# Kernel tuning notes

Measured on AMD Instinct MI355X. Metric: run time of the kernel, lower is better.

The kernel has to match this reference:

```python
import jax, jax.numpy as jnp
import numpy as np

B, Z, H, T = 256, 512, 1024, 512   # batch, z_size, hidden (conductor==decoder), num_tokens
L, N = 16, 16                      # num_levels, notes_per_bar


def setup_inputs() -> dict:
    key = jax.random.key(0)
    ks = jax.random.split(key, 16)
    s = 0.05  # weight init scale
    rn = lambda k, shp, sc=1.0: sc * jax.random.normal(k, shp, dtype=jnp.float32)
    return {
        "z": rn(ks[0], (B, L * N, 1, Z)),
        "dec_h0": rn(ks[1], (L, B, H)),
        "dec_c0": rn(ks[2], (L, B, H)),
        # linear_in (computed but unused by the original forward)
        "lin_in_W": rn(ks[3], (Z, Z), s), "lin_in_b": rn(ks[4], (Z,), s),
        # conductor LSTM (input Z -> hidden H), PyTorch gate order i,f,g,o
        "cond_Wih": rn(ks[5], (4 * H, Z), s), "cond_Whh": rn(ks[6], (4 * H, H), s),
        "cond_bih": rn(ks[7], (4 * H,), s), "cond_bhh": rn(ks[8], (4 * H,), s),
        # decoder LSTM (input T+H -> hidden H)
        "dec_Wih": rn(ks[9], (4 * H, T + H), s), "dec_Whh": rn(ks[10], (4 * H, H), s),
        "dec_bih": rn(ks[11], (4 * H,), s), "dec_bhh": rn(ks[12], (4 * H,), s),
        # output projection
        "out_W": rn(ks[13], (T, H), s), "out_b": rn(ks[14], (T,), s),
    }


def _lstm_cell(x, h, c, Wih, Whh, b):
    gates = x @ Wih.T + h @ Whh.T + b            # [B, 4H]
    i, f, g, o = jnp.split(gates, 4, axis=-1)
    c = jax.nn.sigmoid(f) * c + jax.nn.sigmoid(i) * jnp.tanh(g)
    h = jax.nn.sigmoid(o) * jnp.tanh(c)
    return h, c


def reference(z, dec_h0, dec_c0, lin_in_W, lin_in_b,
              cond_Wih, cond_Whh, cond_bih, cond_bhh,
              dec_Wih, dec_Whh, dec_bih, dec_bhh, out_W, out_b):
    Bsz = z.shape[0]
    Tt = out_b.shape[0]
    Hh = cond_Whh.shape[1]

    _unused = z @ lin_in_W.T + lin_in_b  # linear_in output is discarded in the source

    cond_b = cond_bih + cond_bhh
    dec_b = dec_bih + dec_bhh

    # conductor consumes z[:, L*level, 0, :] for each level
    z_lv = jnp.transpose(z[:, jnp.arange(L) * L, 0, :], (1, 0, 2))  # [L, B, Z]

    def level_step(carry, xs):
        ch, cc = carry
        zl, dh, dc = xs
        ch, cc = _lstm_cell(zl, ch, cc, cond_Wih, cond_Whh, cond_b)
        emb = ch  # [B, H], fixed conductor embedding for this bar

        def note_step(c2, _):
            note, dh2, dc2 = c2
            inp = jnp.concatenate([emb, note], axis=-1)  # [B, H+T]
            dh2, dc2 = _lstm_cell(inp, dh2, dc2, dec_Wih, dec_Whh, dec_b)
            out = jax.nn.sigmoid(dh2 @ out_W.T + out_b)  # [B, T]
            return (out, dh2, dc2), out

        note0 = jnp.zeros((Bsz, Tt), dtype=z.dtype)
        _, outs = jax.lax.scan(note_step, (note0, dh, dc), None, length=N)  # [N, B, T]
        return (ch, cc), outs

    h0 = jnp.zeros((Bsz, Hh), dtype=z.dtype)
    _, all_outs = jax.lax.scan(level_step, (h0, h0), (z_lv, dec_h0, dec_c0))  # [L, N, B, T]
    notes = jnp.transpose(all_outs, (2, 0, 1, 3)).reshape(Bsz, L * N, Tt)
    return notes
```

## Files before the change

### kernel.cpp

```cpp
#include <hip/hip_runtime.h>

typedef __bf16 bf16;
typedef __attribute__((ext_vector_type(8))) __bf16 bf16x8;
typedef __attribute__((ext_vector_type(4))) float f32x4;
typedef __attribute__((ext_vector_type(4))) unsigned short u16x4;

__device__ __forceinline__ void gload_lds16(const void* g, void* l) {
  __builtin_amdgcn_global_load_lds(
      (const __attribute__((address_space(1))) void*)g,
      (__attribute__((address_space(3))) void*)l, 16, 0, 0);
}

__device__ __forceinline__ float sigmoidf_(float x) { return 1.0f / (1.0f + expf(-x)); }

__device__ __forceinline__ float bf2f(unsigned short u) {
  union { unsigned int i; float f; } v;
  v.i = ((unsigned int)u) << 16;
  return v.f;
}
__device__ __forceinline__ unsigned short f2bfbits(float x) {
  union { bf16 b; unsigned short u; } v;
  v.b = (bf16)x;
  return v.u;
}

#define SB() __builtin_amdgcn_sched_barrier(0)
#define BAR()                          \
  do {                                 \
    SB();                              \
    __builtin_amdgcn_s_barrier();      \
    SB();                              \
  } while (0)

#define MFMA16(a, b, c) __builtin_amdgcn_mfma_f32_16x16x32_bf16(a, b, c, 0, 0, 0)

template<int MODE>
__global__ __launch_bounds__(512, 2)
void gemm8(const bf16* __restrict__ A, int lda,
           const bf16* __restrict__ Bw, int K,
           bf16* __restrict__ Cb,
           const bf16* __restrict__ X, const float* __restrict__ bias,
           float* __restrict__ cst, bf16* __restrict__ hout, int ldh) {
  extern __shared__ __align__(16) char smem_raw[];
  bf16* lsA = (bf16*)smem_raw;
  bf16* lsB = lsA + 2 * 16384;

  const int tid = threadIdx.x;
  const int lane = tid & 63;
  const int wave = tid >> 6;
  const int wm = wave >> 2, wn = wave & 3;

  const int bid = blockIdx.x;
  const int wgid = (bid & 7) * 32 + (bid >> 3);
  const int m0 = (wgid >> 4) * 256, n0 = (wgid & 15) * 256;

  const int nkt = K >> 6;

  const int srow = tid >> 3;
  const int csw = ((tid & 7) * 8) ^ ((srow & 7) << 3);
  const bf16* gA = A + (size_t)m0 * lda + csw;
  const bf16* gB = Bw + (size_t)n0 * K + csw;

  auto stageA = [&](int kt) {
    bf16* d = lsA + (kt & 1) * 16384 + tid * 8;
    const bf16* s = gA + (size_t)srow * lda + (size_t)kt * 64;
    gload_lds16(s, d);
    gload_lds16(s + (size_t)64 * lda, d + 4096);
    gload_lds16(s + (size_t)128 * lda, d + 8192);
    gload_lds16(s + (size_t)192 * lda, d + 12288);
  };
  auto stageB = [&](int kt) {
    bf16* d = lsB + (kt & 1) * 16384 + tid * 8;
    const bf16* s = gB + (size_t)srow * K + (size_t)kt * 64;
    gload_lds16(s, d);
    gload_lds16(s + (size_t)64 * K, d + 4096);
    gload_lds16(s + (size_t)128 * K, d + 8192);
    gload_lds16(s + (size_t)192 * K, d + 12288);
  };

  const int c0 = ((lane >> 4) * 8) ^ ((lane & 7) << 3);
  const int c1 = c0 ^ 32;
  const int abase = (wm * 128 + (lane & 15)) * 64;
  const int bbase = (wn * 64 + (lane & 15)) * 64;

  f32x4 acc[8][4] = {};

  stageA(0); stageB(0);
  if (nkt > 1) stageB(1);
  if (nkt > 1) asm volatile("s_waitcnt vmcnt(4)" ::: "memory");
  else         asm volatile("s_waitcnt vmcnt(0)" ::: "memory");
  BAR();

  for (int u = 0; u < nkt; ++u) {
    const int c = u & 1;
    const bf16* pA = lsA + c * 16384;
    const bf16* pB = lsB + c * 16384;
    bf16x8 avA[4], avB[4], avC[4], avD[4], bvA[4], bvB[4];

    if (u + 1 < nkt) stageA(u + 1);
#pragma unroll
    for (int f = 0; f < 4; ++f) avA[f] = *(const bf16x8*)&pA[abase + f * 1024 + c0];
#pragma unroll
    for (int g = 0; g < 4; ++g) bvA[g] = *(const bf16x8*)&pB[bbase + g * 1024 + c0];
#pragma unroll
    for (int f = 0; f < 4; ++f) avB[f] = *(const bf16x8*)&pA[abase + (f + 4) * 1024 + c0];
    BAR();
    __builtin_amdgcn_s_setprio(1);
#pragma unroll
    for (int f = 0; f < 4; ++f)
#pragma unroll
      for (int g = 0; g < 4; ++g)
        acc[f][g] = MFMA16(avA[f], bvA[g], acc[f][g]);
    __builtin_amdgcn_s_setprio(0);
    BAR();

#pragma unroll
    for (int f = 0; f < 4; ++f) avC[f] = *(const bf16x8*)&pA[abase + f * 1024 + c1];
#pragma unroll
    for (int g = 0; g < 4; ++g) bvB[g] = *(const bf16x8*)&pB[bbase + g * 1024 + c1];
    __builtin_amdgcn_s_setprio(1);
#pragma unroll
    for (int f = 0; f < 4; ++f)
#pragma unroll
      for (int g = 0; g < 4; ++g)
        acc[f + 4][g] = MFMA16(avB[f], bvA[g], acc[f + 4][g]);
    __builtin_amdgcn_s_setprio(0);
    BAR();

#pragma unroll
    for (int f = 0; f < 4; ++f) avD[f] = *(const bf16x8*)&pA[abase + (f + 4) * 1024 + c1];
    __builtin_amdgcn_s_setprio(1);
#pragma unroll
    for (int f = 0; f < 4; ++f)
#pragma unroll
      for (int g = 0; g < 4; ++g)
        acc[f][g] = MFMA16(avC[f], bvB[g], acc[f][g]);
    __builtin_amdgcn_s_setprio(0);
    BAR();

    if (u + 2 < nkt) stageB(u + 2);
    SB();
    __builtin_amdgcn_s_setprio(1);
#pragma unroll
    for (int f = 0; f < 4; ++f)
#pragma unroll
      for (int g = 0; g < 4; ++g)
        acc[f + 4][g] = MFMA16(avD[f], bvB[g], acc[f + 4][g]);
    __builtin_amdgcn_s_setprio(0);
    if (u + 2 < nkt)      asm volatile("s_waitcnt vmcnt(4)" ::: "memory");
    else if (u + 1 < nkt) asm volatile("s_waitcnt vmcnt(0)" ::: "memory");
    BAR();
  }

  const int jj = lane & 15;
  const int rb = m0 + wm * 128 + ((lane >> 4) << 2);
  const int q = (n0 >> 6) + wn;
  if constexpr (MODE == 0) {
#pragma unroll
    for (int f = 0; f < 8; ++f)
#pragma unroll
      for (int r = 0; r < 4; ++r) {
        u16x4 pk;
        pk[0] = f2bfbits(acc[f][0][r]);
        pk[1] = f2bfbits(acc[f][1][r]);
        pk[2] = f2bfbits(acc[f][2][r]);
        pk[3] = f2bfbits(acc[f][3][r]);
        *(u16x4*)&Cb[(size_t)(rb + f * 16 + r) * 4096 + q * 64 + jj * 4] = pk;
      }
  } else {
    const int j = q * 16 + jj;
    const f32x4 bq = *(const f32x4*)&bias[q * 64 + jj * 4];
#pragma unroll
    for (int f = 0; f < 8; ++f) {
#pragma unroll
      for (int r = 0; r < 4; ++r) {
        const int row = rb + f * 16 + r;
        const u16x4 xv = *(const u16x4*)&X[(size_t)row * 4096 + q * 64 + jj * 4];
        const float gi = acc[f][0][r] + bf2f(xv[0]) + bq[0];
        const float gf = acc[f][1][r] + bf2f(xv[1]) + bq[1];
        const float gg = acc[f][2][r] + bf2f(xv[2]) + bq[2];
        const float go = acc[f][3][r] + bf2f(xv[3]) + bq[3];
        const size_t ci = (size_t)row * 1024 + j;
        const float cn = sigmoidf_(gf) * cst[ci] + sigmoidf_(gi) * tanhf(gg);
        cst[ci] = cn;
        hout[(size_t)row * ldh + j] = (bf16)(sigmoidf_(go) * tanhf(cn));
      }
    }
  }
}

template<int BM, int BN, int WM, int WN, int MODE>
__global__ __launch_bounds__(WM * WN * 64)
void gemm_bt(const bf16* __restrict__ A, int lda,
             const bf16* __restrict__ Bw, int ldb,
             float* __restrict__ C, int ldc, int K,
             const float* __restrict__ outb, float* __restrict__ dout,
             bf16* __restrict__ anote, int nstep) {
  constexpr int BK = 64;
  constexpr int THREADS = WM * WN * 64;
  constexpr int SM = BM / WM, SN = BN / WN;
  constexpr int FM = SM / 16, FN = SN / 16;

  __shared__ __align__(16) bf16 lsA[BM * BK];
  __shared__ __align__(16) bf16 lsB[BN * BK];

  const int tid = threadIdx.x;
  const int lane = tid & 63;
  const int wave = tid >> 6;
  const int wm = wave / WN, wn = wave % WN;
  const int m0 = blockIdx.y * BM;
  const int n0 = blockIdx.x * BN;

  f32x4 acc[FM][FN] = {};

  const bf16* gA = A + (size_t)m0 * lda;
  const bf16* gB = Bw + (size_t)n0 * ldb;

  for (int k0 = 0; k0 < K; k0 += BK) {
#pragma unroll
    for (int i = 0; i < (BM * 8) / THREADS; ++i) {
      int idx = i * THREADS + tid;
      gload_lds16(gA + (size_t)(idx >> 3) * lda + k0 + (idx & 7) * 8, &lsA[idx * 8]);
    }
#pragma unroll
    for (int i = 0; i < (BN * 8) / THREADS; ++i) {
      int idx = i * THREADS + tid;
      gload_lds16(gB + (size_t)(idx >> 3) * ldb + k0 + (idx & 7) * 8, &lsB[idx * 8]);
    }
    __syncthreads();

#pragma unroll
    for (int kk = 0; kk < BK; kk += 32) {
      bf16x8 av[FM], bv[FN];
#pragma unroll
      for (int i = 0; i < FM; ++i)
        av[i] = *(const bf16x8*)&lsA[(wm * SM + i * 16 + (lane & 15)) * BK + kk + (lane >> 4) * 8];
#pragma unroll
      for (int j = 0; j < FN; ++j)
        bv[j] = *(const bf16x8*)&lsB[(wn * SN + j * 16 + (lane & 15)) * BK + kk + (lane >> 4) * 8];
#pragma unroll
      for (int i = 0; i < FM; ++i)
#pragma unroll
        for (int j = 0; j < FN; ++j)
          acc[i][j] = MFMA16(av[i], bv[j], acc[i][j]);
    }
    __syncthreads();
  }

#pragma unroll
  for (int i = 0; i < FM; ++i) {
#pragma unroll
    for (int j = 0; j < FN; ++j) {
      const int col = n0 + wn * SN + j * 16 + (lane & 15);
      const int rbase = m0 + wm * SM + i * 16 + ((lane >> 4) << 2);
#pragma unroll
      for (int r = 0; r < 4; ++r) {
        const int row = rbase + r;
        float v = acc[i][j][r];
        if constexpr (MODE == 0) {
          C[(size_t)row * ldc + col] = v;
        } else {
          v = sigmoidf_(v + outb[col]);
          const int l = row >> 8, b = row & 255;
          dout[((size_t)(b * 256 + l * 16 + nstep)) * 512 + col] = v;
          anote[(size_t)row * 1536 + col] = (bf16)v;
        }
      }
    }
  }
}

template<int BM, int BJ, int WM, int WJ>
__global__ __launch_bounds__(WM * WJ * 64, 2)
void gemm_cell(const bf16* __restrict__ A, int lda,
               const bf16* __restrict__ Bw,
               const bf16* __restrict__ X,
               const float* __restrict__ bias,
               float* __restrict__ cst,
               bf16* __restrict__ hout, int ldh, int K) {
  constexpr int BK = 64;
  constexpr int THREADS = WM * WJ * 64;
  constexpr int BN = BJ * 64;
  constexpr int SM = BM / WM;
  constexpr int TJ = BJ / WJ;
  constexpr int FM = SM / 16;

  __shared__ __align__(16) bf16 lsA[BM * BK];
  __shared__ __align__(16) bf16 lsB[BN * BK];

  const int tid = threadIdx.x;
  const int lane = tid & 63;
  const int wave = tid >> 6;
  const int wm = wave / WJ, wj = wave % WJ;
  const int m0 = blockIdx.y * BM;
  const int qb = blockIdx.x * BJ;

  f32x4 acc[FM][TJ][4] = {};

  const bf16* gA = A + (size_t)m0 * lda;
  const bf16* gB = Bw + (size_t)(qb * 64) * K;

  for (int k0 = 0; k0 < K; k0 += BK) {
#pragma unroll
    for (int i = 0; i < (BM * 8) / THREADS; ++i) {
      int idx = i * THREADS + tid;
      gload_lds16(gA + (size_t)(idx >> 3) * lda + k0 + (idx & 7) * 8, &lsA[idx * 8]);
    }
#pragma unroll
    for (int i = 0; i < (BN * 8) / THREADS; ++i) {
      int idx = i * THREADS + tid;
      gload_lds16(gB + (size_t)(idx >> 3) * K + k0 + (idx & 7) * 8, &lsB[idx * 8]);
    }
    __syncthreads();

#pragma unroll
    for (int kk = 0; kk < BK; kk += 32) {
      bf16x8 av[FM], bv[TJ][4];
#pragma unroll
      for (int i = 0; i < FM; ++i)
        av[i] = *(const bf16x8*)&lsA[(wm * SM + i * 16 + (lane & 15)) * BK + kk + (lane >> 4) * 8];
#pragma unroll
      for (int t = 0; t < TJ; ++t)
#pragma unroll
        for (int g = 0; g < 4; ++g)
          bv[t][g] = *(const bf16x8*)
              &lsB[((wj * TJ + t) * 64 + g * 16 + (lane & 15)) * BK + kk + (lane >> 4) * 8];
#pragma unroll
      for (int i = 0; i < FM; ++i)
#pragma unroll
        for (int t = 0; t < TJ; ++t)
#pragma unroll
          for (int g = 0; g < 4; ++g)
            acc[i][t][g] = MFMA16(av[i], bv[t][g], acc[i][t][g]);
    }
    __syncthreads();
  }

#pragma unroll
  for (int i = 0; i < FM; ++i) {
#pragma unroll
    for (int t = 0; t < TJ; ++t) {
      const int q = qb + wj * TJ + t;
      const int jj = lane & 15;
      const int j = q * 16 + jj;
      const int rbase = m0 + wm * SM + i * 16 + ((lane >> 4) << 2);
      const f32x4 bq = *(const f32x4*)&bias[q * 64 + jj * 4];
#pragma unroll
      for (int r = 0; r < 4; ++r) {
        const int row = rbase + r;
        const u16x4 xv = *(const u16x4*)&X[(size_t)row * 4096 + q * 64 + jj * 4];
        const float gi = acc[i][t][0][r] + bf2f(xv[0]) + bq[0];
        const float gf = acc[i][t][1][r] + bf2f(xv[1]) + bq[1];
        const float gg = acc[i][t][2][r] + bf2f(xv[2]) + bq[2];
        const float go = acc[i][t][3][r] + bf2f(xv[3]) + bq[3];
        const size_t ci = (size_t)row * 1024 + j;
        const float c = sigmoidf_(gf) * cst[ci] + sigmoidf_(gi) * tanhf(gg);
        cst[ci] = c;
        hout[(size_t)row * ldh + j] = (bf16)(sigmoidf_(go) * tanhf(c));
      }
    }
  }
}


__global__ void conv_f32_bf16(const float* __restrict__ src, bf16* __restrict__ dst, int n) {
  int idx = blockIdx.x * 256 + threadIdx.x;
  if (idx < n) dst[idx] = (bf16)src[idx];
}

__device__ __forceinline__ int p_src_row(int n) {
  int q = n >> 6, gate = (n >> 4) & 3, jj = n & 15;
  return gate * 1024 + q * 16 + jj;
}

__global__ void pack_w_dec(const float* __restrict__ wih, const float* __restrict__ whh,
                           bf16* __restrict__ dst) {
  int idx = blockIdx.x * 256 + threadIdx.x;
  int n = idx / 1536, c = idx - n * 1536;
  int r = p_src_row(n);
  float v = (c < 512) ? wih[(size_t)r * 1536 + 1024 + c] : whh[(size_t)r * 1024 + (c - 512)];
  dst[idx] = (bf16)v;
}

__global__ void pack_w_emb(const float* __restrict__ wih, bf16* __restrict__ dst) {
  int idx = blockIdx.x * 256 + threadIdx.x;
  int n = idx >> 10, c = idx & 1023;
  dst[idx] = (bf16)wih[(size_t)p_src_row(n) * 1536 + c];
}

__global__ void pack_w_perm(const float* __restrict__ src, bf16* __restrict__ dst, int Kw) {
  int idx = blockIdx.x * 256 + threadIdx.x;
  int n = idx / Kw, c = idx - n * Kw;
  dst[idx] = (bf16)src[(size_t)p_src_row(n) * Kw + c];
}

__global__ void pack_bias(const float* __restrict__ bih, const float* __restrict__ bhh,
                          float* __restrict__ dst) {
  int n = blockIdx.x * 256 + threadIdx.x;
  int q = n >> 6, jj = (n >> 2) & 15, g = n & 3;
  int r = g * 1024 + q * 16 + jj;
  dst[n] = bih[r] + bhh[r];
}

__global__ void pack_zb(const float* __restrict__ z, bf16* __restrict__ dst) {
  int idx = blockIdx.x * 256 + threadIdx.x;
  int m = idx >> 9, k = idx & 511;
  int l = m >> 8, b = m & 255;
  dst[idx] = (bf16)z[((size_t)b * 256 + 16 * l) * 512 + k];
}

__global__ void init_cond(float* __restrict__ cc, bf16* __restrict__ hz0) {
  int idx = blockIdx.x * 256 + threadIdx.x;
  cc[idx] = 0.f;
  hz0[idx] = (bf16)0.f;
}

__global__ void init_state(const float* __restrict__ h0, const float* __restrict__ c0,
                           bf16* __restrict__ Abuf, float* __restrict__ cdec) {
  int idx = blockIdx.x * 256 + threadIdx.x;
  int m = idx / 1536, c = idx - m * 1536;
  if (c < 512) {
    Abuf[idx] = (bf16)0.f;
  } else {
    int j = c - 512;
    size_t s = (size_t)m * 1024 + j;
    Abuf[idx] = (bf16)h0[s];
    cdec[s] = c0[s];
  }
}

extern "C" void kernel_launch(void* const* d_in, const int* in_sizes, int n_in,
                              void* d_out, int out_size, void* d_ws, size_t ws_size,
                              hipStream_t stream) {
  const float* z        = (const float*)d_in[0];
  const float* dec_h0   = (const float*)d_in[1];
  const float* dec_c0   = (const float*)d_in[2];
  const float* cond_Wih = (const float*)d_in[5];
  const float* cond_Whh = (const float*)d_in[6];
  const float* cond_bih = (const float*)d_in[7];
  const float* cond_bhh = (const float*)d_in[8];
  const float* dec_Wih  = (const float*)d_in[9];
  const float* dec_Whh  = (const float*)d_in[10];
  const float* dec_bih  = (const float*)d_in[11];
  const float* dec_bhh  = (const float*)d_in[12];
  const float* out_W    = (const float*)d_in[13];
  const float* out_b    = (const float*)d_in[14];
  float* out = (float*)d_out;

  char* ws = (char*)d_ws;
  size_t off = 0;
  auto alloc = [&](size_t bytes) {
    void* p = ws + off;
    off += (bytes + 255) & ~(size_t)255;
    return p;
  };
  bf16* E     = (bf16*)alloc(4096ull * 4096 * 2);
  bf16* Xz    = (bf16*)alloc(4096ull * 4096 * 2);
  float* cdec = (float*)alloc(4096ull * 1024 * 4);
  bf16* Abuf  = (bf16*)alloc(4096ull * 1536 * 2);
  bf16* Wd    = (bf16*)alloc(4096ull * 1536 * 2);
  bf16* We    = (bf16*)alloc(4096ull * 1024 * 2);
  bf16* Wcih  = (bf16*)alloc(4096ull * 512 * 2);
  bf16* Wchh  = (bf16*)alloc(4096ull * 1024 * 2);
  bf16* Wo    = (bf16*)alloc(512ull * 1024 * 2);
  float* cc   = (float*)alloc(256ull * 1024 * 4);
  bf16* emb   = (bf16*)alloc(4096ull * 1024 * 2);
  bf16* Zb    = (bf16*)alloc(4096ull * 512 * 2);
  bf16* hz0   = (bf16*)alloc(256ull * 1024 * 2);
  float* bdP  = (float*)alloc(4096ull * 4);
  float* bcP  = (float*)alloc(4096ull * 4);

  dim3 b256(256);

  hipFuncSetAttribute(reinterpret_cast<const void*>(&gemm8<0>),
                      hipFuncAttributeMaxDynamicSharedMemorySize, 131072);
  hipFuncSetAttribute(reinterpret_cast<const void*>(&gemm8<1>),
                      hipFuncAttributeMaxDynamicSharedMemorySize, 131072);

  pack_w_perm<<<4096 * 512 / 256, b256, 0, stream>>>(cond_Wih, Wcih, 512);
  pack_w_perm<<<4096 * 1024 / 256, b256, 0, stream>>>(cond_Whh, Wchh, 1024);
  conv_f32_bf16<<<(512 * 1024 + 255) / 256, b256, 0, stream>>>(out_W, Wo, 512 * 1024);
  pack_w_dec<<<4096 * 1536 / 256, b256, 0, stream>>>(dec_Wih, dec_Whh, Wd);
  pack_w_emb<<<4096 * 1024 / 256, b256, 0, stream>>>(dec_Wih, We);
  pack_bias<<<16, b256, 0, stream>>>(dec_bih, dec_bhh, bdP);
  pack_bias<<<16, b256, 0, stream>>>(cond_bih, cond_bhh, bcP);
  pack_zb<<<4096 * 512 / 256, b256, 0, stream>>>(z, Zb);
  init_cond<<<256 * 1024 / 256, b256, 0, stream>>>(cc, hz0);
  init_state<<<4096 * 1536 / 256, b256, 0, stream>>>(dec_h0, dec_c0, Abuf, cdec);

  gemm8<0><<<256, 512, 131072, stream>>>(Zb, 512, Wcih, 512, Xz,
                                         nullptr, nullptr, nullptr, nullptr, 0);

  for (int l = 0; l < 16; ++l) {
    const bf16* hprev = (l == 0) ? hz0 : (emb + (size_t)(l - 1) * 256 * 1024);
    gemm_cell<32, 2, 2, 2><<<dim3(32, 8), dim3(256), 0, stream>>>(
        hprev, 1024, Wchh, Xz + (size_t)l * 256 * 4096, bcP,
        cc, emb + (size_t)l * 256 * 1024, 1024, 1024);
  }

  gemm8<0><<<256, 512, 131072, stream>>>(emb, 1024, We, 1024, E,
                                         nullptr, nullptr, nullptr, nullptr, 0);

  for (int n = 0; n < 16; ++n) {
    gemm8<1><<<256, 512, 131072, stream>>>(Abuf, 1536, Wd, 1536, nullptr,
                                           E, bdP, cdec, Abuf + 512, 1536);
    gemm_bt<128, 64, 2, 2, 1><<<dim3(512 / 64, 4096 / 128), dim3(256), 0, stream>>>(
        Abuf + 512, 1536, Wo, 1024, nullptr, 0, 1024, out_b, out, Abuf, n);
  }
}
```

Measured before the change: 1.750 ms.

## Restage gemm8 into K-half phases with one barrier each; ping-pong decoder state

The gemm8 main loop is rebuilt. Shared memory now holds each 64-wide K tile as two unswizzled 32-wide halves. Each loop iteration covers two K tiles in four phases, and each phase has one barrier, a full 8x4 MFMA block, and an async global-to-LDS prefetch of a later half. This replaces four barriers per K tile with one per half-tile and gives longer uninterrupted MFMA runs. The decoder step loop also alternates between two state buffers, so gemm8<1> no longer writes the new hidden state into the same buffer it is reading, removing a cross-block hazard at the cost of one extra workspace buffer. The loop assumes an even number of K tiles and relies on tight vmcnt accounting to stay correct.

```diff
diff --git a/kernel.cpp b/kernel.cpp
--- a/kernel.cpp
+++ b/kernel.cpp
@@ -25,13 +25,6 @@
 }
 
 #define SB() __builtin_amdgcn_sched_barrier(0)
-#define BAR()                          \
-  do {                                 \
-    SB();                              \
-    __builtin_amdgcn_s_barrier();      \
-    SB();                              \
-  } while (0)
-
 #define MFMA16(a, b, c) __builtin_amdgcn_mfma_f32_16x16x32_bf16(a, b, c, 0, 0, 0)
 
 template<int MODE>
@@ -43,7 +36,7 @@
            float* __restrict__ cst, bf16* __restrict__ hout, int ldh) {
   extern __shared__ __align__(16) char smem_raw[];
   bf16* lsA = (bf16*)smem_raw;
-  bf16* lsB = lsA + 2 * 16384;
+  bf16* lsB = lsA + 32768;
 
   const int tid = threadIdx.x;
   const int lane = tid & 63;
@@ -56,101 +49,85 @@
 
   const int nkt = K >> 6;
 
-  const int srow = tid >> 3;
-  const int csw = ((tid & 7) * 8) ^ ((srow & 7) << 3);
-  const bf16* gA = A + (size_t)m0 * lda + csw;
-  const bf16* gB = Bw + (size_t)n0 * K + csw;
-
-  auto stageA = [&](int kt) {
-    bf16* d = lsA + (kt & 1) * 16384 + tid * 8;
-    const bf16* s = gA + (size_t)srow * lda + (size_t)kt * 64;
+  const int srow = tid >> 2;
+  const int scol = (tid & 3) * 8;
+  const bf16* gAs = A + (size_t)(m0 + srow) * lda + scol;
+  const bf16* gBs = Bw + (size_t)(n0 + srow) * K + scol;
+
+  auto stA = [&](int kt, int ks) {
+    bf16* d = lsA + (kt & 1) * 16384 + ks * 8192 + tid * 8;
+    const bf16* s = gAs + (size_t)kt * 64 + ks * 32;
     gload_lds16(s, d);
-    gload_lds16(s + (size_t)64 * lda, d + 4096);
-    gload_lds16(s + (size_t)128 * lda, d + 8192);
-    gload_lds16(s + (size_t)192 * lda, d + 12288);
+    gload_lds16(s + (size_t)128 * lda, d + 4096);
   };
-  auto stageB = [&](int kt) {
-    bf16* d = lsB + (kt & 1) * 16384 + tid * 8;
-    const bf16* s = gB + (size_t)srow * K + (size_t)kt * 64;
+  auto stB = [&](int kt, int ks) {
+    bf16* d = lsB + (kt & 1) * 16384 + ks * 8192 + tid * 8;
+    const bf16* s = gBs + (size_t)kt * 64 + ks * 32;
     gload_lds16(s, d);
-    gload_lds16(s + (size_t)64 * K, d + 4096);
-    gload_lds16(s + (size_t)128 * K, d + 8192);
-    gload_lds16(s + (size_t)192 * K, d + 12288);
+    gload_lds16(s + (size_t)128 * K, d + 4096);
   };
 
-  const int c0 = ((lane >> 4) * 8) ^ ((lane & 7) << 3);
-  const int c1 = c0 ^ 32;
-  const int abase = (wm * 128 + (lane & 15)) * 64;
-  const int bbase = (wn * 64 + (lane & 15)) * 64;
+  const int aoff = (wm * 128 + (lane & 15)) * 32 + (lane >> 4) * 8;
+  const int boff = (wn * 64 + (lane & 15)) * 32 + (lane >> 4) * 8;
 
   f32x4 acc[8][4] = {};
 
-  stageA(0); stageB(0);
-  if (nkt > 1) stageB(1);
-  if (nkt > 1) asm volatile("s_waitcnt vmcnt(4)" ::: "memory");
-  else         asm volatile("s_waitcnt vmcnt(0)" ::: "memory");
-  BAR();
-
-  for (int u = 0; u < nkt; ++u) {
-    const int c = u & 1;
-    const bf16* pA = lsA + c * 16384;
-    const bf16* pB = lsB + c * 16384;
-    bf16x8 avA[4], avB[4], avC[4], avD[4], bvA[4], bvB[4];
-
-    if (u + 1 < nkt) stageA(u + 1);
-#pragma unroll
-    for (int f = 0; f < 4; ++f) avA[f] = *(const bf16x8*)&pA[abase + f * 1024 + c0];
-#pragma unroll
-    for (int g = 0; g < 4; ++g) bvA[g] = *(const bf16x8*)&pB[bbase + g * 1024 + c0];
-#pragma unroll
-    for (int f = 0; f < 4; ++f) avB[f] = *(const bf16x8*)&pA[abase + (f + 4) * 1024 + c0];
-    BAR();
-    __builtin_amdgcn_s_setprio(1);
-#pragma unroll
-    for (int f = 0; f < 4; ++f)
-#pragma unroll
-      for (int g = 0; g < 4; ++g)
-        acc[f][g] = MFMA16(avA[f], bvA[g], acc[f][g]);
-    __builtin_amdgcn_s_setprio(0);
-    BAR();
-
-#pragma unroll
-    for (int f = 0; f < 4; ++f) avC[f] = *(const bf16x8*)&pA[abase + f * 1024 + c1];
-#pragma unroll
-    for (int g = 0; g < 4; ++g) bvB[g] = *(const bf16x8*)&pB[bbase + g * 1024 + c1];
-    __builtin_amdgcn_s_setprio(1);
-#pragma unroll
-    for (int f = 0; f < 4; ++f)
-#pragma unroll
-      for (int g = 0; g < 4; ++g)
-        acc[f + 4][g] = MFMA16(avB[f], bvA[g], acc[f + 4][g]);
-    __builtin_amdgcn_s_setprio(0);
-    BAR();
-
-#pragma unroll
-    for (int f = 0; f < 4; ++f) avD[f] = *(const bf16x8*)&pA[abase + (f + 4) * 1024 + c1];
-    __builtin_amdgcn_s_setprio(1);
-#pragma unroll
-    for (int f = 0; f < 4; ++f)
-#pragma unroll
-      for (int g = 0; g < 4; ++g)
-        acc[f][g] = MFMA16(avC[f], bvB[g], acc[f][g]);
-    __builtin_amdgcn_s_setprio(0);
-    BAR();
-
-    if (u + 2 < nkt) stageB(u + 2);
-    SB();
-    __builtin_amdgcn_s_setprio(1);
-#pragma unroll
-    for (int f = 0; f < 4; ++f)
-#pragma unroll
-      for (int g = 0; g < 4; ++g)
-        acc[f + 4][g] = MFMA16(avD[f], bvB[g], acc[f + 4][g]);
-    __builtin_amdgcn_s_setprio(0);
-    if (u + 2 < nkt)      asm volatile("s_waitcnt vmcnt(4)" ::: "memory");
-    else if (u + 1 < nkt) asm volatile("s_waitcnt vmcnt(0)" ::: "memory");
-    BAR();
-  }
+  stA(0, 0); stB(0, 0);
+  stA(0, 1); stB(0, 1);
+  stA(1, 0); stB(1, 0);
+  asm volatile("s_waitcnt vmcnt(8)" ::: "memory");
+
+#define PHASE(REGION_A, REGION_B, STAGE_STMT, WAIT_STMT)                      \
+  do {                                                                        \
+    SB();                                                                     \
+    __builtin_amdgcn_s_barrier();                                             \
+    SB();                                                                     \
+    bf16x8 av[8], bv[4];                                                      \
+    _Pragma("unroll")                                                         \
+    for (int f = 0; f < 8; ++f)                                               \
+      av[f] = *(const bf16x8*)&(REGION_A)[aoff + f * 512];                    \
+    _Pragma("unroll")                                                         \
+    for (int g = 0; g < 4; ++g)                                               \
+      bv[g] = *(const bf16x8*)&(REGION_B)[boff + g * 512];                    \
+    STAGE_STMT;                                                               \
+    asm volatile("s_waitcnt lgkmcnt(0)" ::: "memory");                        \
+    SB();                                                                     \
+    __builtin_amdgcn_s_setprio(1);                                            \
+    _Pragma("unroll")                                                         \
+    for (int f = 0; f < 8; ++f)                                               \
+      _Pragma("unroll")                                                       \
+      for (int g = 0; g < 4; ++g)                                             \
+        acc[f][g] = MFMA16(av[f], bv[g], acc[f][g]);                          \
+    __builtin_amdgcn_s_setprio(0);                                            \
+    WAIT_STMT;                                                                \
+  } while (0)
+
+  for (int t = 0; t < nkt; t += 2) {
+    const bool pre = (t + 2 < nkt);
+    const bf16* A00 = lsA;
+    const bf16* A01 = lsA + 8192;
+    const bf16* A10 = lsA + 16384;
+    const bf16* A11 = lsA + 24576;
+    const bf16* B00 = lsB;
+    const bf16* B01 = lsB + 8192;
+    const bf16* B10 = lsB + 16384;
+    const bf16* B11 = lsB + 24576;
+
+    PHASE(A00, B00,
+          { stA(t + 1, 1); stB(t + 1, 1); },
+          { if (pre) asm volatile("s_waitcnt vmcnt(8)" ::: "memory");
+            else     asm volatile("s_waitcnt vmcnt(0)" ::: "memory"); });
+    PHASE(A01, B01,
+          { if (pre) { stA(t + 2, 0); stB(t + 2, 0); } },
+          { if (pre) asm volatile("s_waitcnt vmcnt(8)" ::: "memory"); });
+    PHASE(A10, B10,
+          { if (pre) { stA(t + 2, 1); stB(t + 2, 1); } },
+          { if (pre) asm volatile("s_waitcnt vmcnt(8)" ::: "memory"); });
+    PHASE(A11, B11,
+          { if (pre) { stA(t + 3, 0); stB(t + 3, 0); } },
+          { if (pre) asm volatile("s_waitcnt vmcnt(8)" ::: "memory"); });
+  }
+#undef PHASE
 
   const int jj = lane & 15;
   const int rb = m0 + wm * 128 + ((lane >> 4) << 2);
@@ -457,7 +434,8 @@
   bf16* E     = (bf16*)alloc(4096ull * 4096 * 2);
   bf16* Xz    = (bf16*)alloc(4096ull * 4096 * 2);
   float* cdec = (float*)alloc(4096ull * 1024 * 4);
-  bf16* Abuf  = (bf16*)alloc(4096ull * 1536 * 2);
+  bf16* Ab0   = (bf16*)alloc(4096ull * 1536 * 2);
+  bf16* Ab1   = (bf16*)alloc(4096ull * 1536 * 2);
   bf16* Wd    = (bf16*)alloc(4096ull * 1536 * 2);
   bf16* We    = (bf16*)alloc(4096ull * 1024 * 2);
   bf16* Wcih  = (bf16*)alloc(4096ull * 512 * 2);
@@ -486,7 +464,7 @@
   pack_bias<<<16, b256, 0, stream>>>(cond_bih, cond_bhh, bcP);
   pack_zb<<<4096 * 512 / 256, b256, 0, stream>>>(z, Zb);
   init_cond<<<256 * 1024 / 256, b256, 0, stream>>>(cc, hz0);
-  init_state<<<4096 * 1536 / 256, b256, 0, stream>>>(dec_h0, dec_c0, Abuf, cdec);
+  init_state<<<4096 * 1536 / 256, b256, 0, stream>>>(dec_h0, dec_c0, Ab0, cdec);
 
   gemm8<0><<<256, 512, 131072, stream>>>(Zb, 512, Wcih, 512, Xz,
                                          nullptr, nullptr, nullptr, nullptr, 0);
@@ -502,9 +480,11 @@
                                          nullptr, nullptr, nullptr, nullptr, 0);
 
   for (int n = 0; n < 16; ++n) {
-    gemm8<1><<<256, 512, 131072, stream>>>(Abuf, 1536, Wd, 1536, nullptr,
-                                           E, bdP, cdec, Abuf + 512, 1536);
+    bf16* Sc = (n & 1) ? Ab1 : Ab0;
+    bf16* Sn = (n & 1) ? Ab0 : Ab1;
+    gemm8<1><<<256, 512, 131072, stream>>>(Sc, 1536, Wd, 1536, nullptr,
+                                           E, bdP, cdec, Sn + 512, 1536);
     gemm_bt<128, 64, 2, 2, 1><<<dim3(512 / 64, 4096 / 128), dim3(256), 0, stream>>>(
-        Abuf + 512, 1536, Wo, 1024, nullptr, 0, 1024, out_b, out, Abuf, n);
-  }
-}
+        Sn + 512, 1536, Wo, 1024, nullptr, 0, 1024, out_b, out, Sn, n);
+  }
+}
```

Result: no change. 1.757 ms (+0.4%).
